# Kernel optimization log

Measured on AMD Instinct MI355X. Metric: run time of the kernel, lower is better.

## Reference

```python
import jax, jax.numpy as jnp
import numpy as np

B, S, D, H = 2, 2048, 1024, 16
HD = D // H  # 64
NUM_BUCKETS = 32
MAX_DISTANCE = 128


def _relative_position_bucket(relative_position, num_buckets=NUM_BUCKETS, max_distance=MAX_DISTANCE):
    # bidirectional=True branch of the torch code
    num_buckets //= 2
    rel_buckets = (relative_position > 0).astype(jnp.int32) * num_buckets
    rp = jnp.abs(relative_position)
    max_exact = num_buckets // 2
    is_small = rp < max_exact
    # log-spaced buckets for larger distances
    rp_large = max_exact + (
        jnp.log(rp.astype(jnp.float32) / max_exact)
        / np.log(max_distance / max_exact)
        * (num_buckets - max_exact)
    ).astype(jnp.int32)
    rp_large = jnp.minimum(rp_large, num_buckets - 1)
    return rel_buckets + jnp.where(is_small, rp, rp_large)


def compute_bias(rel_bias, query_length, key_length):
    ctx = jnp.arange(query_length)[:, None]
    mem = jnp.arange(key_length)[None, :]
    buckets = _relative_position_bucket(mem - ctx)  # [q, k]
    values = rel_bias[buckets]                      # [q, k, h]
    return jnp.transpose(values, (2, 0, 1))[None]   # [1, h, q, k]


def setup_inputs() -> dict:
    key = jax.random.key(0)
    ks = jax.random.split(key, 6)
    scale = 1.0 / np.sqrt(D)
    return {
        "hidden_states": jax.random.normal(ks[0], (B, S, D), jnp.float32),
        "mask": jnp.ones((B, 1, 1, S), jnp.int32),
        "Wq": jax.random.normal(ks[1], (D, D), jnp.float32) * scale,
        "Wk": jax.random.normal(ks[2], (D, D), jnp.float32) * scale,
        "Wv": jax.random.normal(ks[3], (D, D), jnp.float32) * scale,
        "Wo": jax.random.normal(ks[4], (D, D), jnp.float32) * scale,
        "rel_bias": jax.random.normal(ks[5], (NUM_BUCKETS, H), jnp.float32),
    }


def reference(hidden_states, mask, Wq, Wk, Wv, Wo, rel_bias):
    b, s, _ = hidden_states.shape
    # projections (no bias), split heads -> [b, h, s, hd]
    def proj(x, W):
        return jnp.einsum("bsd,ed->bse", x, W).reshape(b, s, H, HD).transpose(0, 2, 1, 3)
    q = proj(hidden_states, Wq)
    k = proj(hidden_states, Wk)
    v = proj(hidden_states, Wv)
    # unscaled attention scores (T5 style): [b, h, s, s]
    scores = jnp.einsum("bhqd,bhkd->bhqk", q, k)
    position_bias = compute_bias(rel_bias, s, s)
    scores = scores + position_bias
    scores = jnp.where(mask == 0, jnp.float32(-1e9), scores)
    attn_weights = jax.nn.softmax(scores, axis=-1)
    # dropout p=0.0 (eval): identity
    attn_output = jnp.einsum("bhqk,bhkd->bhqd", attn_weights, v)
    attn_output = attn_output.transpose(0, 2, 1, 3).reshape(b, s, H * HD)
    attn_output = jnp.einsum("bse,de->bsd", attn_output, Wo)
    return attn_output, attn_weights, position_bias
```

## Files before the change

### kernel.cpp

```cpp
#include <hip/hip_runtime.h>

typedef __attribute__((ext_vector_type(8))) _Float16 half8;
typedef __attribute__((ext_vector_type(4))) _Float16 half4;
typedef __attribute__((ext_vector_type(4))) float f32x4;

#define SEQ 2048
#define DMODEL 1024
#define NHEAD 16
#define HEADD 64
#define NBH 32
#define LUTW 4096

__device__ __forceinline__ void nt_store_f4(float* p, f32x4 v) {
    __builtin_nontemporal_store(v, (f32x4*)p);
}

#define LDS_BAR() do {                                   \
    __builtin_amdgcn_sched_barrier(0);                   \
    asm volatile("s_waitcnt lgkmcnt(0)" ::: "memory");   \
    __builtin_amdgcn_sched_barrier(0);                   \
    __builtin_amdgcn_s_barrier();                        \
    __builtin_amdgcn_sched_barrier(0);                   \
} while (0)

__device__ __forceinline__ int rel_bucket(int rel) {
    int ret = (rel > 0) ? 16 : 0;
    int rp = rel < 0 ? -rel : rel;
    if (rp < 8) return ret + rp;
    float x = logf((float)rp * 0.125f) / 2.7725887f * 8.0f;
    int v = 8 + (int)x;
    v = v < 15 ? v : 15;
    return ret + v;
}

__global__ __launch_bounds__(256) void prep_kernel(const float* __restrict__ hs,
                                                   const float* __restrict__ Wq,
                                                   const float* __restrict__ Wk,
                                                   const float* __restrict__ Wv,
                                                   const float* __restrict__ Wo,
                                                   const float* __restrict__ rel_bias,
                                                   _Float16* __restrict__ Xh,
                                                   _Float16* __restrict__ Wqh,
                                                   _Float16* __restrict__ Wkh,
                                                   _Float16* __restrict__ Wvh,
                                                   _Float16* __restrict__ Woh,
                                                   float* __restrict__ lut) {
    int bid = blockIdx.x;
    if (bid < 4096) {
        const float* in;
        _Float16* out;
        int base;
        if (bid < 2048)      { in = hs; out = Xh;  base = bid; }
        else if (bid < 2560) { in = Wq; out = Wqh; base = bid - 2048; }
        else if (bid < 3072) { in = Wk; out = Wkh; base = bid - 2560; }
        else if (bid < 3584) { in = Wv; out = Wvh; base = bid - 3072; }
        else                 { in = Wo; out = Woh; base = bid - 3584; }
        int i = (base * 256 + threadIdx.x) * 8;
        f32x4 a = *(const f32x4*)(in + i);
        f32x4 b = *(const f32x4*)(in + i + 4);
        half8 r;
        r[0] = (_Float16)a[0]; r[1] = (_Float16)a[1];
        r[2] = (_Float16)a[2]; r[3] = (_Float16)a[3];
        r[4] = (_Float16)b[0]; r[5] = (_Float16)b[1];
        r[6] = (_Float16)b[2]; r[7] = (_Float16)b[3];
        *(half8*)(out + i) = r;
    } else {
        int i = (bid - 4096) * 256 + threadIdx.x;
        int h = i >> 12;
        int idx = i & (LUTW - 1);
        int rel = idx - 2047;
        int b = rel_bucket(rel);
        lut[i] = rel_bias[b * NHEAD + h];
    }
}

__global__ __launch_bounds__(256) void proj3_kernel(const _Float16* __restrict__ Xh,
                                                    const _Float16* __restrict__ Wqh,
                                                    const _Float16* __restrict__ Wkh,
                                                    const _Float16* __restrict__ Wvh,
                                                    _Float16* __restrict__ Qh,
                                                    _Float16* __restrict__ Kh,
                                                    _Float16* __restrict__ Vt,
                                                    const float* __restrict__ lut,
                                                    float* __restrict__ posb) {
    int z = blockIdx.z;
    if (z == 3) {
        int flat = blockIdx.y * 8 + blockIdx.x;
        const size_t total = (size_t)NHEAD * SEQ * SEQ / 4;
        for (size_t idx = (size_t)flat * 256 + threadIdx.x; idx < total; idx += 65536) {
            size_t e = idx * 4;
            int k = (int)(e & 2047);
            int q = (int)((e >> 11) & 2047);
            int h = (int)(e >> 22);
            f32x4 v;
            __builtin_memcpy(&v, lut + h * LUTW + (k - q + 2047), 16);
            nt_store_f4(posb + e, v);
        }
        return;
    }
    const _Float16* B = (z == 0) ? Wqh : (z == 1) ? Wkh : Wvh;
    int l = threadIdx.x & 63, w = threadIdx.x >> 6;
    int row0 = blockIdx.y * 128 + (w >> 1) * 64;
    int col0 = blockIdx.x * 128 + (w & 1) * 64;
    int ar = l & 15, ak = (l >> 4) * 8;
    f32x4 acc[4][4] = {};
    for (int k0 = 0; k0 < DMODEL; k0 += 32) {
        half8 af[4], bf[4];
#pragma unroll
        for (int mi = 0; mi < 4; mi++)
            af[mi] = *(const half8*)(Xh + (size_t)(row0 + mi * 16 + ar) * DMODEL + k0 + ak);
#pragma unroll
        for (int ni = 0; ni < 4; ni++)
            bf[ni] = *(const half8*)(B + (size_t)(col0 + ni * 16 + ar) * DMODEL + k0 + ak);
#pragma unroll
        for (int mi = 0; mi < 4; mi++)
#pragma unroll
            for (int ni = 0; ni < 4; ni++)
                acc[mi][ni] = __builtin_amdgcn_mfma_f32_16x16x32_f16(af[mi], bf[ni], acc[mi][ni], 0, 0, 0);
    }
    int cr = (l >> 4) * 4, cc = l & 15;
    if (z < 2) {
        _Float16* C = z == 0 ? Qh : Kh;
#pragma unroll
        for (int mi = 0; mi < 4; mi++)
#pragma unroll
            for (int ni = 0; ni < 4; ni++) {
                int c = col0 + ni * 16 + cc;
#pragma unroll
                for (int j = 0; j < 4; j++)
                    C[(size_t)(row0 + mi * 16 + cr + j) * DMODEL + c] = (_Float16)acc[mi][ni][j];
            }
    } else {
#pragma unroll
        for (int mi = 0; mi < 4; mi++)
#pragma unroll
            for (int ni = 0; ni < 4; ni++) {
                int c = col0 + ni * 16 + cc;
                int h = c >> 6, hd = c & 63;
                int r = row0 + mi * 16 + cr;
                int b = r >> 11, s0 = r & 2047;
                half4 pk;
#pragma unroll
                for (int j = 0; j < 4; j++) pk[j] = (_Float16)acc[mi][ni][j];
                *(half4*)(Vt + (size_t)((b * NHEAD + h) * HEADD + hd) * SEQ + s0) = pk;
            }
    }
}

__global__ __launch_bounds__(256) void outgemm_kernel(const _Float16* __restrict__ A,
                                                      const _Float16* __restrict__ B,
                                                      float* __restrict__ C) {
    int l = threadIdx.x & 63, w = threadIdx.x >> 6;
    int row0 = blockIdx.y * 128 + (w >> 1) * 64;
    int col0 = blockIdx.x * 128 + (w & 1) * 64;
    int ar = l & 15, ak = (l >> 4) * 8;
    f32x4 acc[4][4] = {};
    for (int k0 = 0; k0 < DMODEL; k0 += 32) {
        half8 af[4], bf[4];
#pragma unroll
        for (int mi = 0; mi < 4; mi++)
            af[mi] = *(const half8*)(A + (size_t)(row0 + mi * 16 + ar) * DMODEL + k0 + ak);
#pragma unroll
        for (int ni = 0; ni < 4; ni++)
            bf[ni] = *(const half8*)(B + (size_t)(col0 + ni * 16 + ar) * DMODEL + k0 + ak);
#pragma unroll
        for (int mi = 0; mi < 4; mi++)
#pragma unroll
            for (int ni = 0; ni < 4; ni++)
                acc[mi][ni] = __builtin_amdgcn_mfma_f32_16x16x32_f16(af[mi], bf[ni], acc[mi][ni], 0, 0, 0);
    }
    int cr = (l >> 4) * 4, cc = l & 15;
#pragma unroll
    for (int mi = 0; mi < 4; mi++)
#pragma unroll
        for (int ni = 0; ni < 4; ni++) {
            int c = col0 + ni * 16 + cc;
#pragma unroll
            for (int j = 0; j < 4; j++)
                C[(size_t)(row0 + mi * 16 + cr + j) * DMODEL + c] = acc[mi][ni][j];
        }
}

__global__ __launch_bounds__(256) void attn_kernel(const _Float16* __restrict__ Q,
                                                   const _Float16* __restrict__ Kg,
                                                   const _Float16* __restrict__ Vg,
                                                   const float* __restrict__ lut,
                                                   const int* __restrict__ mask,
                                                   float* __restrict__ wts,
                                                   _Float16* __restrict__ attn0) {
    __shared__ _Float16 Kt[64][68];
    __shared__ _Float16 Vl[64][68];
    __shared__ _Float16 Pl[4][16][72];
    int tid = threadIdx.x;
    int l = tid & 63, w = tid >> 6;
    int bid = blockIdx.x;
    int xcd = bid & 7, idx = bid >> 3;
    int bh = (idx >> 5) * 8 + xcd;
    int qblk = idx & 31;
    int b = bh >> 4, h = bh & 15;
    int qbase = qblk * 64 + w * 16;
    size_t hoff = (size_t)(b * SEQ) * DMODEL + h * HEADD;
    int ar = l & 15, g = l >> 4, ak = g * 8;
    const float* luth = lut + h * LUTW;
    float* ob = wts + (size_t)bh * SEQ * SEQ;
    int q = qbase + ar;

    int sr = tid >> 2, sc = (tid & 3) * 16;
    const _Float16* Ksrc = Kg + hoff + sc;
    const _Float16* Vsrc = Vg + ((size_t)bh * HEADD + sr) * SEQ + sc;

    half8 qf[2];
#pragma unroll
    for (int kk = 0; kk < 2; kk++)
        qf[kk] = *(const half8*)(Q + hoff + (size_t)q * DMODEL + kk * 32 + ak);

    half8 s0 = *(const half8*)(Ksrc + (size_t)sr * DMODEL);
    half8 s1 = *(const half8*)(Ksrc + (size_t)sr * DMODEL + 8);
    float m = -3e38f, lsum = 0.f;
    for (int k0 = 0; k0 < SEQ; k0 += 64) {
        *(half8*)&Kt[sr][sc] = s0;
        *(half8*)&Kt[sr][sc + 8] = s1;
        LDS_BAR();
        if (k0 + 64 < SEQ) {
            s0 = *(const half8*)(Ksrc + (size_t)(k0 + 64 + sr) * DMODEL);
            s1 = *(const half8*)(Ksrc + (size_t)(k0 + 64 + sr) * DMODEL + 8);
        }
        f32x4 acc[4] = {};
#pragma unroll
        for (int ni = 0; ni < 4; ni++)
#pragma unroll
            for (int kk = 0; kk < 2; kk++) {
                half8 kf = *(const half8*)&Kt[ni * 16 + ar][kk * 32 + ak];
                acc[ni] = __builtin_amdgcn_mfma_f32_16x16x32_f16(kf, qf[kk], acc[ni], 0, 0, 0);
            }
        LDS_BAR();
        float vv[16];
#pragma unroll
        for (int ni = 0; ni < 4; ni++) {
            int kcol = k0 + ni * 16 + g * 4;
            int4 mk = *(const int4*)(mask + b * SEQ + kcol);
            const int* mp = (const int*)&mk;
            f32x4 lb4;
            __builtin_memcpy(&lb4, luth + kcol - q + 2047, 16);
#pragma unroll
            for (int j = 0; j < 4; j++)
                vv[ni * 4 + j] = mp[j] ? (acc[ni][j] + lb4[j]) : -1e9f;
        }
        float t8[8];
#pragma unroll
        for (int t = 0; t < 8; t++) t8[t] = fmaxf(vv[t], vv[t + 8]);
        float t4a = fmaxf(t8[0], t8[4]), t4b = fmaxf(t8[1], t8[5]);
        float t4c = fmaxf(t8[2], t8[6]), t4d = fmaxf(t8[3], t8[7]);
        float vmax = fmaxf(fmaxf(t4a, t4b), fmaxf(t4c, t4d));
        float mn = fmaxf(m, vmax);
        float scale = __expf(m - mn);
        float e[16];
#pragma unroll
        for (int t = 0; t < 16; t++) e[t] = __expf(vv[t] - mn);
        float s8[8];
#pragma unroll
        for (int t = 0; t < 8; t++) s8[t] = e[t] + e[t + 8];
        float s4a = s8[0] + s8[4], s4b = s8[1] + s8[5];
        float s4c = s8[2] + s8[6], s4d = s8[3] + s8[7];
        float s = (s4a + s4b) + (s4c + s4d);
        lsum = lsum * scale + s;
        m = mn;
    }
    half8 t0 = *(const half8*)(Ksrc + (size_t)sr * DMODEL);
    half8 t1 = *(const half8*)(Ksrc + (size_t)sr * DMODEL + 8);
    half8 v0 = *(const half8*)(Vsrc);
    half8 v1 = *(const half8*)(Vsrc + 8);
#pragma unroll
    for (int off2 = 16; off2 <= 32; off2 <<= 1) {
        float mo = __shfl_xor(m, off2);
        float lo = __shfl_xor(lsum, off2);
        float mn = fmaxf(m, mo);
        lsum = lsum * __expf(m - mn) + lo * __expf(mo - mn);
        m = mn;
    }
    float invl = 1.0f / lsum;
    LDS_BAR();

    f32x4 oacc[4] = {};
    for (int k0 = 0; k0 < SEQ; k0 += 64) {
        *(half8*)&Kt[sr][sc] = t0;
        *(half8*)&Kt[sr][sc + 8] = t1;
        *(half8*)&Vl[sr][sc] = v0;
        *(half8*)&Vl[sr][sc + 8] = v1;
        LDS_BAR();
        if (k0 + 64 < SEQ) {
            t0 = *(const half8*)(Ksrc + (size_t)(k0 + 64 + sr) * DMODEL);
            t1 = *(const half8*)(Ksrc + (size_t)(k0 + 64 + sr) * DMODEL + 8);
            v0 = *(const half8*)(Vsrc + k0 + 64);
            v1 = *(const half8*)(Vsrc + k0 + 64 + 8);
        }
        f32x4 acc[4] = {};
#pragma unroll
        for (int ni = 0; ni < 4; ni++)
#pragma unroll
            for (int kk = 0; kk < 2; kk++) {
                half8 kf = *(const half8*)&Kt[ni * 16 + ar][kk * 32 + ak];
                acc[ni] = __builtin_amdgcn_mfma_f32_16x16x32_f16(kf, qf[kk], acc[ni], 0, 0, 0);
            }
#pragma unroll
        for (int ni = 0; ni < 4; ni++) {
            int kcol = k0 + ni * 16 + g * 4;
            int4 mk = *(const int4*)(mask + b * SEQ + kcol);
            const int* mp = (const int*)&mk;
            f32x4 lb4;
            __builtin_memcpy(&lb4, luth + kcol - q + 2047, 16);
            f32x4 wv;
#pragma unroll
            for (int j = 0; j < 4; j++) {
                float v = mp[j] ? (acc[ni][j] + lb4[j]) : -1e9f;
                wv[j] = __expf(v - m) * invl;
            }
            nt_store_f4(ob + (size_t)q * SEQ + kcol, wv);
            half4 ph;
#pragma unroll
            for (int j = 0; j < 4; j++) ph[j] = (_Float16)wv[j];
            *(half4*)&Pl[w][ar][ni * 16 + g * 4] = ph;
        }
#pragma unroll
        for (int kk2 = 0; kk2 < 2; kk2++) {
            half8 pa = *(half8*)&Pl[w][ar][kk2 * 32 + g * 8];
#pragma unroll
            for (int ni = 0; ni < 4; ni++) {
                half8 vf = *(const half8*)&Vl[ni * 16 + ar][kk2 * 32 + g * 8];
                oacc[ni] = __builtin_amdgcn_mfma_f32_16x16x32_f16(pa, vf, oacc[ni], 0, 0, 0);
            }
        }
        LDS_BAR();
    }
#pragma unroll
    for (int ni = 0; ni < 4; ni++)
#pragma unroll
        for (int j = 0; j < 4; j++)
            attn0[(size_t)(b * SEQ + qbase + g * 4 + j) * DMODEL + h * HEADD + ni * 16 + ar] =
                (_Float16)oacc[ni][j];
}

extern "C" void kernel_launch(void* const* d_in, const int* in_sizes, int n_in,
                              void* d_out, int out_size, void* d_ws, size_t ws_size,
                              hipStream_t stream) {
    const float* hs = (const float*)d_in[0];
    const int* mask = (const int*)d_in[1];
    const float* Wq = (const float*)d_in[2];
    const float* Wk = (const float*)d_in[3];
    const float* Wv = (const float*)d_in[4];
    const float* Wo = (const float*)d_in[5];
    const float* rel_bias = (const float*)d_in[6];

    float* out_attn = (float*)d_out;
    float* out_wts = out_attn + (size_t)2 * SEQ * DMODEL;
    float* out_posb = out_wts + (size_t)NBH * SEQ * SEQ;

    char* ws = (char*)d_ws;
    size_t off = 0;
    auto carve = [&](size_t bytes) { void* p = ws + off; off += (bytes + 255) & ~(size_t)255; return p; };
    _Float16* Xh  = (_Float16*)carve((size_t)2 * SEQ * DMODEL * 2);
    _Float16* Wqh = (_Float16*)carve((size_t)DMODEL * DMODEL * 2);
    _Float16* Wkh = (_Float16*)carve((size_t)DMODEL * DMODEL * 2);
    _Float16* Wvh = (_Float16*)carve((size_t)DMODEL * DMODEL * 2);
    _Float16* Woh = (_Float16*)carve((size_t)DMODEL * DMODEL * 2);
    _Float16* Qh  = (_Float16*)carve((size_t)2 * SEQ * DMODEL * 2);
    _Float16* Kh  = (_Float16*)carve((size_t)2 * SEQ * DMODEL * 2);
    _Float16* Vt  = (_Float16*)carve((size_t)NBH * HEADD * SEQ * 2);
    _Float16* A0h = (_Float16*)carve((size_t)2 * SEQ * DMODEL * 2);
    float* lut    = (float*)carve((size_t)NHEAD * LUTW * 4);

    prep_kernel<<<4352, 256, 0, stream>>>(hs, Wq, Wk, Wv, Wo, rel_bias,
                                          Xh, Wqh, Wkh, Wvh, Woh, lut);

    dim3 pg(DMODEL / 128, (2 * SEQ) / 128, 4);
    proj3_kernel<<<pg, 256, 0, stream>>>(Xh, Wqh, Wkh, Wvh, Qh, Kh, Vt, lut, out_posb);

    attn_kernel<<<1024, 256, 0, stream>>>(Qh, Kh, Vt, lut, mask, out_wts, A0h);

    dim3 og(DMODEL / 128, (2 * SEQ) / 128);
    outgemm_kernel<<<og, 256, 0, stream>>>(A0h, Woh, out_attn);
}
```

Measured before the change: 454.4 us.

## Process two query tiles per block, fusing second tile's stats pass into first's output pass

Each block now handles two 64-row query tiles (A and B, 1024 rows apart) and launches half as many blocks. Tile B's row max/sum pass is folded into tile A's output pass so both reuse the same K tile loaded into LDS. This cuts the K streaming from four passes per two tiles to three. In exchange, register pressure rises and parallelism halves to 512 blocks of 256 threads, which may leave CUs underutilised on a 256-CU part.

```diff
diff --git a/kernel.cpp b/kernel.cpp
--- a/kernel.cpp
+++ b/kernel.cpp
@@ -195,28 +195,32 @@
     int l = tid & 63, w = tid >> 6;
     int bid = blockIdx.x;
     int xcd = bid & 7, idx = bid >> 3;
-    int bh = (idx >> 5) * 8 + xcd;
-    int qblk = idx & 31;
+    int bh = (idx >> 4) * 8 + xcd;
+    int qpair = idx & 15;
     int b = bh >> 4, h = bh & 15;
-    int qbase = qblk * 64 + w * 16;
+    int qbaseA = qpair * 64 + w * 16;
+    int qbaseB = qbaseA + 1024;
     size_t hoff = (size_t)(b * SEQ) * DMODEL + h * HEADD;
     int ar = l & 15, g = l >> 4, ak = g * 8;
     const float* luth = lut + h * LUTW;
     float* ob = wts + (size_t)bh * SEQ * SEQ;
-    int q = qbase + ar;
+    int qA = qbaseA + ar;
+    int qB = qbaseB + ar;
 
     int sr = tid >> 2, sc = (tid & 3) * 16;
     const _Float16* Ksrc = Kg + hoff + sc;
     const _Float16* Vsrc = Vg + ((size_t)bh * HEADD + sr) * SEQ + sc;
 
-    half8 qf[2];
-#pragma unroll
-    for (int kk = 0; kk < 2; kk++)
-        qf[kk] = *(const half8*)(Q + hoff + (size_t)q * DMODEL + kk * 32 + ak);
+    half8 qfA[2], qfB[2];
+#pragma unroll
+    for (int kk = 0; kk < 2; kk++) {
+        qfA[kk] = *(const half8*)(Q + hoff + (size_t)qA * DMODEL + kk * 32 + ak);
+        qfB[kk] = *(const half8*)(Q + hoff + (size_t)qB * DMODEL + kk * 32 + ak);
+    }
 
     half8 s0 = *(const half8*)(Ksrc + (size_t)sr * DMODEL);
     half8 s1 = *(const half8*)(Ksrc + (size_t)sr * DMODEL + 8);
-    float m = -3e38f, lsum = 0.f;
+    float mA = -3e38f, lsumA = 0.f;
     for (int k0 = 0; k0 < SEQ; k0 += 64) {
         *(half8*)&Kt[sr][sc] = s0;
         *(half8*)&Kt[sr][sc + 8] = s1;
@@ -231,7 +235,7 @@
 #pragma unroll
             for (int kk = 0; kk < 2; kk++) {
                 half8 kf = *(const half8*)&Kt[ni * 16 + ar][kk * 32 + ak];
-                acc[ni] = __builtin_amdgcn_mfma_f32_16x16x32_f16(kf, qf[kk], acc[ni], 0, 0, 0);
+                acc[ni] = __builtin_amdgcn_mfma_f32_16x16x32_f16(kf, qfA[kk], acc[ni], 0, 0, 0);
             }
         LDS_BAR();
         float vv[16];
@@ -241,7 +245,7 @@
             int4 mk = *(const int4*)(mask + b * SEQ + kcol);
             const int* mp = (const int*)&mk;
             f32x4 lb4;
-            __builtin_memcpy(&lb4, luth + kcol - q + 2047, 16);
+            __builtin_memcpy(&lb4, luth + kcol - qA + 2047, 16);
 #pragma unroll
             for (int j = 0; j < 4; j++)
                 vv[ni * 4 + j] = mp[j] ? (acc[ni][j] + lb4[j]) : -1e9f;
@@ -252,8 +256,8 @@
         float t4a = fmaxf(t8[0], t8[4]), t4b = fmaxf(t8[1], t8[5]);
         float t4c = fmaxf(t8[2], t8[6]), t4d = fmaxf(t8[3], t8[7]);
         float vmax = fmaxf(fmaxf(t4a, t4b), fmaxf(t4c, t4d));
-        float mn = fmaxf(m, vmax);
-        float scale = __expf(m - mn);
+        float mn = fmaxf(mA, vmax);
+        float scale = __expf(mA - mn);
         float e[16];
 #pragma unroll
         for (int t = 0; t < 16; t++) e[t] = __expf(vv[t] - mn);
@@ -262,9 +266,8 @@
         for (int t = 0; t < 8; t++) s8[t] = e[t] + e[t + 8];
         float s4a = s8[0] + s8[4], s4b = s8[1] + s8[5];
         float s4c = s8[2] + s8[6], s4d = s8[3] + s8[7];
-        float s = (s4a + s4b) + (s4c + s4d);
-        lsum = lsum * scale + s;
-        m = mn;
+        lsumA = lsumA * scale + (s4a + s4b) + (s4c + s4d);
+        mA = mn;
     }
     half8 t0 = *(const half8*)(Ksrc + (size_t)sr * DMODEL);
     half8 t1 = *(const half8*)(Ksrc + (size_t)sr * DMODEL + 8);
@@ -272,16 +275,17 @@
     half8 v1 = *(const half8*)(Vsrc + 8);
 #pragma unroll
     for (int off2 = 16; off2 <= 32; off2 <<= 1) {
-        float mo = __shfl_xor(m, off2);
-        float lo = __shfl_xor(lsum, off2);
-        float mn = fmaxf(m, mo);
-        lsum = lsum * __expf(m - mn) + lo * __expf(mo - mn);
-        m = mn;
-    }
-    float invl = 1.0f / lsum;
+        float mo = __shfl_xor(mA, off2);
+        float lo = __shfl_xor(lsumA, off2);
+        float mn = fmaxf(mA, mo);
+        lsumA = lsumA * __expf(mA - mn) + lo * __expf(mo - mn);
+        mA = mn;
+    }
+    float invlA = 1.0f / lsumA;
     LDS_BAR();
 
-    f32x4 oacc[4] = {};
+    f32x4 oaccA[4] = {};
+    float mB = -3e38f, lsumB = 0.f;
     for (int k0 = 0; k0 < SEQ; k0 += 64) {
         *(half8*)&Kt[sr][sc] = t0;
         *(half8*)&Kt[sr][sc + 8] = t1;
@@ -294,13 +298,14 @@
             v0 = *(const half8*)(Vsrc + k0 + 64);
             v1 = *(const half8*)(Vsrc + k0 + 64 + 8);
         }
-        f32x4 acc[4] = {};
+        f32x4 accA[4] = {}, accB[4] = {};
 #pragma unroll
         for (int ni = 0; ni < 4; ni++)
 #pragma unroll
             for (int kk = 0; kk < 2; kk++) {
                 half8 kf = *(const half8*)&Kt[ni * 16 + ar][kk * 32 + ak];
-                acc[ni] = __builtin_amdgcn_mfma_f32_16x16x32_f16(kf, qf[kk], acc[ni], 0, 0, 0);
+                accA[ni] = __builtin_amdgcn_mfma_f32_16x16x32_f16(kf, qfA[kk], accA[ni], 0, 0, 0);
+                accB[ni] = __builtin_amdgcn_mfma_f32_16x16x32_f16(kf, qfB[kk], accB[ni], 0, 0, 0);
             }
 #pragma unroll
         for (int ni = 0; ni < 4; ni++) {
@@ -308,14 +313,118 @@
             int4 mk = *(const int4*)(mask + b * SEQ + kcol);
             const int* mp = (const int*)&mk;
             f32x4 lb4;
-            __builtin_memcpy(&lb4, luth + kcol - q + 2047, 16);
+            __builtin_memcpy(&lb4, luth + kcol - qA + 2047, 16);
+            f32x4 wv;
+#pragma unroll
+            for (int j = 0; j < 4; j++) {
+                float v = mp[j] ? (accA[ni][j] + lb4[j]) : -1e9f;
+                wv[j] = __expf(v - mA) * invlA;
+            }
+            nt_store_f4(ob + (size_t)qA * SEQ + kcol, wv);
+            half4 ph;
+#pragma unroll
+            for (int j = 0; j < 4; j++) ph[j] = (_Float16)wv[j];
+            *(half4*)&Pl[w][ar][ni * 16 + g * 4] = ph;
+        }
+#pragma unroll
+        for (int kk2 = 0; kk2 < 2; kk2++) {
+            half8 pa = *(half8*)&Pl[w][ar][kk2 * 32 + g * 8];
+#pragma unroll
+            for (int ni = 0; ni < 4; ni++) {
+                half8 vf = *(const half8*)&Vl[ni * 16 + ar][kk2 * 32 + g * 8];
+                oaccA[ni] = __builtin_amdgcn_mfma_f32_16x16x32_f16(pa, vf, oaccA[ni], 0, 0, 0);
+            }
+        }
+        {
+            float vv[16];
+#pragma unroll
+            for (int ni = 0; ni < 4; ni++) {
+                int kcol = k0 + ni * 16 + g * 4;
+                int4 mk = *(const int4*)(mask + b * SEQ + kcol);
+                const int* mp = (const int*)&mk;
+                f32x4 lb4;
+                __builtin_memcpy(&lb4, luth + kcol - qB + 2047, 16);
+#pragma unroll
+                for (int j = 0; j < 4; j++)
+                    vv[ni * 4 + j] = mp[j] ? (accB[ni][j] + lb4[j]) : -1e9f;
+            }
+            float t8[8];
+#pragma unroll
+            for (int t = 0; t < 8; t++) t8[t] = fmaxf(vv[t], vv[t + 8]);
+            float t4a = fmaxf(t8[0], t8[4]), t4b = fmaxf(t8[1], t8[5]);
+            float t4c = fmaxf(t8[2], t8[6]), t4d = fmaxf(t8[3], t8[7]);
+            float vmax = fmaxf(fmaxf(t4a, t4b), fmaxf(t4c, t4d));
+            float mn = fmaxf(mB, vmax);
+            float scale = __expf(mB - mn);
+            float e[16];
+#pragma unroll
+            for (int t = 0; t < 16; t++) e[t] = __expf(vv[t] - mn);
+            float s8[8];
+#pragma unroll
+            for (int t = 0; t < 8; t++) s8[t] = e[t] + e[t + 8];
+            float s4a = s8[0] + s8[4], s4b = s8[1] + s8[5];
+            float s4c = s8[2] + s8[6], s4d = s8[3] + s8[7];
+            lsumB = lsumB * scale + (s4a + s4b) + (s4c + s4d);
+            mB = mn;
+        }
+        LDS_BAR();
+    }
+#pragma unroll
+    for (int ni = 0; ni < 4; ni++)
+#pragma unroll
+        for (int j = 0; j < 4; j++)
+            attn0[(size_t)(b * SEQ + qbaseA + g * 4 + j) * DMODEL + h * HEADD + ni * 16 + ar] =
+                (_Float16)oaccA[ni][j];
+    half8 u0 = *(const half8*)(Ksrc + (size_t)sr * DMODEL);
+    half8 u1 = *(const half8*)(Ksrc + (size_t)sr * DMODEL + 8);
+    half8 w0 = *(const half8*)(Vsrc);
+    half8 w1 = *(const half8*)(Vsrc + 8);
+#pragma unroll
+    for (int off2 = 16; off2 <= 32; off2 <<= 1) {
+        float mo = __shfl_xor(mB, off2);
+        float lo = __shfl_xor(lsumB, off2);
+        float mn = fmaxf(mB, mo);
+        lsumB = lsumB * __expf(mB - mn) + lo * __expf(mo - mn);
+        mB = mn;
+    }
+    float invlB = 1.0f / lsumB;
+    LDS_BAR();
+
+    f32x4 oaccB[4] = {};
+    for (int k0 = 0; k0 < SEQ; k0 += 64) {
+        *(half8*)&Kt[sr][sc] = u0;
+        *(half8*)&Kt[sr][sc + 8] = u1;
+        *(half8*)&Vl[sr][sc] = w0;
+        *(half8*)&Vl[sr][sc + 8] = w1;
+        LDS_BAR();
+        if (k0 + 64 < SEQ) {
+            u0 = *(const half8*)(Ksrc + (size_t)(k0 + 64 + sr) * DMODEL);
+            u1 = *(const half8*)(Ksrc + (size_t)(k0 + 64 + sr) * DMODEL + 8);
+            w0 = *(const half8*)(Vsrc + k0 + 64);
+            w1 = *(const half8*)(Vsrc + k0 + 64 + 8);
+        }
+        f32x4 acc[4] = {};
+#pragma unroll
+        for (int ni = 0; ni < 4; ni++)
+#pragma unroll
+            for (int kk = 0; kk < 2; kk++) {
+                half8 kf = *(const half8*)&Kt[ni * 16 + ar][kk * 32 + ak];
+                acc[ni] = __builtin_amdgcn_mfma_f32_16x16x32_f16(kf, qfB[kk], acc[ni], 0, 0, 0);
+            }
+#pragma unroll
+        for (int ni = 0; ni < 4; ni++) {
+            int kcol = k0 + ni * 16 + g * 4;
+            int4 mk = *(const int4*)(mask + b * SEQ + kcol);
+            const int* mp = (const int*)&mk;
+            f32x4 lb4;
+            __builtin_memcpy(&lb4, luth + kcol - qB + 2047, 16);
             f32x4 wv;
 #pragma unroll
             for (int j = 0; j < 4; j++) {
                 float v = mp[j] ? (acc[ni][j] + lb4[j]) : -1e9f;
-                wv[j] = __expf(v - m) * invl;
-            }
-            nt_store_f4(ob + (size_t)q * SEQ + kcol, wv);
+                wv[j] = __expf(v - mB) * invlB;
+            }
+            nt_store_f4(ob + (size_t)qB * SEQ + kcol, wv);
             half4 ph;
 #pragma unroll
             for (int j = 0; j < 4; j++) ph[j] = (_Float16)wv[j];
@@ -327,7 +436,7 @@
 #pragma unroll
             for (int ni = 0; ni < 4; ni++) {
                 half8 vf = *(const half8*)&Vl[ni * 16 + ar][kk2 * 32 + g * 8];
-                oacc[ni] = __builtin_amdgcn_mfma_f32_16x16x32_f16(pa, vf, oacc[ni], 0, 0, 0);
+                oaccB[ni] = __builtin_amdgcn_mfma_f32_16x16x32_f16(pa, vf, oaccB[ni], 0, 0, 0);
             }
         }
         LDS_BAR();
@@ -336,8 +445,8 @@
     for (int ni = 0; ni < 4; ni++)
 #pragma unroll
         for (int j = 0; j < 4; j++)
-            attn0[(size_t)(b * SEQ + qbase + g * 4 + j) * DMODEL + h * HEADD + ni * 16 + ar] =
-                (_Float16)oacc[ni][j];
+            attn0[(size_t)(b * SEQ + qbaseB + g * 4 + j) * DMODEL + h * HEADD + ni * 16 + ar] =
+                (_Float16)oaccB[ni][j];
 }
 
 extern "C" void kernel_launch(void* const* d_in, const int* in_sizes, int n_in,
@@ -375,7 +484,7 @@
     dim3 pg(DMODEL / 128, (2 * SEQ) / 128, 4);
     proj3_kernel<<<pg, 256, 0, stream>>>(Xh, Wqh, Wkh, Wvh, Qh, Kh, Vt, lut, out_posb);
 
-    attn_kernel<<<1024, 256, 0, stream>>>(Qh, Kh, Vt, lut, mask, out_wts, A0h);
+    attn_kernel<<<512, 256, 0, stream>>>(Qh, Kh, Vt, lut, mask, out_wts, A0h);
 
     dim3 og(DMODEL / 128, (2 * SEQ) / 128);
     outgemm_kernel<<<og, 256, 0, stream>>>(A0h, Woh, out_attn);
```

New measurement: 442.7 us. -2.6%, faster.
